# Kernel tuning notes

Measured on AMD Instinct MI355X. Metric: run time of the kernel, lower is better.

The kernel has to match this reference:

```python
import jax, jax.numpy as jnp
import numpy as np
import math

B, L = 512, 32768
NUM_C, NUM_D = 16, 8
RECIPTIVE, STRIDES = 512, 256
EPS = 1e-4


def setup_inputs() -> dict:
    key = jax.random.key(0)
    kx, kw = jax.random.split(key)
    x = jax.random.normal(kx, (B, L), dtype=jnp.float32)
    stdv = 1.0 / math.sqrt(RECIPTIVE)
    weight = jax.random.uniform(kw, (NUM_C, NUM_D, RECIPTIVE), dtype=jnp.float32,
                                minval=-stdv, maxval=stdv)
    return {"x": x, "weight": weight}


def reference(x, weight):
    # x: [B, L], weight: [C, D, R]
    Lx = x.shape[1]
    # sigma = (W W^T + eps I)^{-1} per capsule, [C, D, D]
    wc = jnp.einsum('cdr,cer->cde', weight, weight)
    sigma = jnp.linalg.inv(wc + EPS * jnp.eye(NUM_D, dtype=weight.dtype))
    # circular sliding windows: [W, R] index map (wraparound matches torch.cat branch)
    starts = jnp.arange(0, Lx, STRIDES)
    idx = (starts[:, None] + jnp.arange(RECIPTIVE)[None, :]) % Lx
    windows = x[:, idx]                                   # [B, W, R]
    proj = jnp.einsum('cdr,bwr->bwcd', weight, windows)    # [B, W, C, D]
    q = jnp.einsum('bwcd,cde,bwce->bwc', proj, sigma, proj)  # quadratic form
    return jnp.mean(jnp.sqrt(q), axis=1)                   # [B, C]
```

## Files before the change

### kernel.cpp

```cpp
#include <hip/hip_runtime.h>
#include <hip/hip_bf16.h>

#define NUM_C  16
#define NUM_D  8
#define RECEPT 512
#define LROW   32768
#define EPS_V  1e-4f

#define XCHUNKS 2112
#define XBYTES  (XCHUNKS * 16)

typedef __attribute__((ext_vector_type(8))) short short8;
typedef __attribute__((ext_vector_type(4))) float f32x4;

__device__ __forceinline__ unsigned short f2bf(float f) {
    unsigned int u = __builtin_bit_cast(unsigned int, f);
    u += 0x7fffu + ((u >> 16) & 1u);
    return (unsigned short)(u >> 16);
}

__device__ __forceinline__ int bsw(int a) { return a ^ (((a >> 11) & 7) << 4); }

__device__ __forceinline__ short8 cvt8(f32x4 lo, f32x4 hi) {
    union { short8 s; __hip_bfloat162 h[4]; } u;
    u.h[0] = __float22bfloat162_rn(make_float2(lo[0], lo[1]));
    u.h[1] = __float22bfloat162_rn(make_float2(lo[2], lo[3]));
    u.h[2] = __float22bfloat162_rn(make_float2(hi[0], hi[1]));
    u.h[3] = __float22bfloat162_rn(make_float2(hi[2], hi[3]));
    return u.s;
}

__global__ void prep_kernel(const float* __restrict__ weight,
                            unsigned short* __restrict__ wfrag,
                            float* __restrict__ out) {
    __shared__ float Wc[NUM_D * RECEPT];
    __shared__ float G[NUM_D][NUM_D];
    __shared__ float Lm[NUM_D][NUM_D];
    const int c = blockIdx.x;
    const int t = threadIdx.x;

    out[c * 256 + t] = 0.f;
    out[c * 256 + t + 4096] = 0.f;

    const float4* wsrc4 = reinterpret_cast<const float4*>(
        weight + (size_t)c * NUM_D * RECEPT);
    float4* Wc4 = reinterpret_cast<float4*>(Wc);
    #pragma unroll
    for (int i = 0; i < 4; ++i) Wc4[t + i * 256] = wsrc4[t + i * 256];
    __syncthreads();

    if (t < 64) {
        int d = t >> 3, e = t & 7;
        const float4* wd4 = reinterpret_cast<const float4*>(&Wc[d * RECEPT]);
        const float4* we4 = reinterpret_cast<const float4*>(&Wc[e * RECEPT]);
        float s = 0.f;
        #pragma unroll 4
        for (int r4 = 0; r4 < RECEPT / 4; ++r4) {
            float4 a = wd4[r4], bb = we4[r4];
            s += a.x * bb.x + a.y * bb.y + a.z * bb.z + a.w * bb.w;
        }
        if (d == e) s += EPS_V;
        G[d][e] = s;
    }
    __syncthreads();
    if (t == 0) {
        for (int i = 0; i < NUM_D; ++i) {
            float diag = G[i][i];
            for (int k = 0; k < i; ++k) diag -= Lm[i][k] * Lm[i][k];
            float di = sqrtf(diag);
            Lm[i][i] = di;
            float inv = 1.f / di;
            for (int jj = i + 1; jj < NUM_D; ++jj) {
                float s = G[jj][i];
                for (int k = 0; k < i; ++k) s -= Lm[jj][k] * Lm[i][k];
                Lm[jj][i] = s * inv;
            }
        }
    }
    __syncthreads();
    for (int r = t; r < RECEPT; r += 256) {
        float y[NUM_D];
        for (int d = 0; d < NUM_D; ++d) {
            float s = Wc[d * RECEPT + r];
            for (int k = 0; k < d; ++k) s -= Lm[d][k] * y[k];
            y[d] = s / Lm[d][d];
        }
        const int kk = r >> 5;
        const int g  = (r >> 3) & 3;
        const int j  = r & 7;
        for (int d = 0; d < NUM_D; ++d) {
            int cd = c * NUM_D + d;
            int ntile = cd >> 4;
            int nl = cd & 15;
            int lane = g * 16 + nl;
            int idx = (((ntile * 16 + kk) * 64) + lane) * 8 + j;
            wfrag[idx] = f2bf(y[d]);
        }
    }
}

__global__ __launch_bounds__(256, 4) void main_kernel(
        const float* __restrict__ x,
        const unsigned short* __restrict__ wfrag,
        float* __restrict__ out) {
    __shared__ char lds[XBYTES];
    const int bid = blockIdx.x;
    const int b  = bid >> 2;
    const int qr = bid & 3;
    const int t = threadIdx.x;
    const int lane = t & 63;
    const int wv = t >> 6;
    const int rl = lane & 15;
    const int gl = lane >> 4;
    const int nt0 = wv * 2;

    const char* slice = (const char*)(x + (size_t)b * LROW + qr * 8192);

    #pragma unroll
    for (int i = 0; i < 8; ++i) {
        const int cb = i * 256 + wv * 64;
        const int q = cb + lane;
        const int sq = q ^ ((q >> 7) & 7);
        __builtin_amdgcn_global_load_lds(
            (const __attribute__((address_space(1))) unsigned int*)(slice + sq * 16),
            (__attribute__((address_space(3))) unsigned int*)(lds + cb * 16),
            16, 0, 0);
    }
    if (wv == 0) {
        const char* tsrc = (qr == 3) ? (const char*)(x + (size_t)b * LROW)
                                     : slice + 32768;
        __builtin_amdgcn_global_load_lds(
            (const __attribute__((address_space(1))) unsigned int*)(tsrc + lane * 16),
            (__attribute__((address_space(3))) unsigned int*)(lds + 32768),
            16, 0, 0);
    }

    f32x4 acc[2][2];
    #pragma unroll
    for (int mi = 0; mi < 2; ++mi)
        #pragma unroll
        for (int ni = 0; ni < 2; ++ni)
            acc[mi][ni] = (f32x4){0.f, 0.f, 0.f, 0.f};

    __syncthreads();

    #pragma unroll 1
    for (int q = 0; q < 4; ++q) {
        short8 bq[4][2];
        #pragma unroll
        for (int kkq = 0; kkq < 4; ++kkq)
            #pragma unroll
            for (int ni = 0; ni < 2; ++ni)
                bq[kkq][ni] = *reinterpret_cast<const short8*>(
                    wfrag + ((size_t)(((nt0 + ni) * 16 + q * 4 + kkq) * 64 + lane)) * 8);

        #pragma unroll
        for (int kkq = 0; kkq < 4; ++kkq) {
            short8 af[2];
            #pragma unroll
            for (int mi = 0; mi < 2; ++mi) {
                const int a0 = (mi * 16 + rl) * 1024 + (q * 4 + kkq) * 128 + gl * 32;
                f32x4 lo = *reinterpret_cast<const f32x4*>(lds + bsw(a0));
                f32x4 hi = *reinterpret_cast<const f32x4*>(lds + bsw(a0 + 16));
                af[mi] = cvt8(lo, hi);
            }
            #pragma unroll
            for (int mi = 0; mi < 2; ++mi) {
                acc[mi][0] = __builtin_amdgcn_mfma_f32_16x16x32_bf16(af[mi], bq[kkq][0], acc[mi][0], 0, 0, 0);
                acc[mi][1] = __builtin_amdgcn_mfma_f32_16x16x32_bf16(af[mi], bq[kkq][1], acc[mi][1], 0, 0, 0);
            }
        }
    }

    #pragma unroll
    for (int ni = 0; ni < 2; ++ni) {
        float s = 0.f;
        #pragma unroll
        for (int mi = 0; mi < 2; ++mi) {
            #pragma unroll
            for (int r = 0; r < 4; ++r) {
                float p = acc[mi][ni][r];
                float qq = p * p;
                qq += __shfl_xor(qq, 1);
                qq += __shfl_xor(qq, 2);
                qq += __shfl_xor(qq, 4);
                s += sqrtf(qq);
            }
        }
        s += __shfl_xor(s, 16);
        s += __shfl_xor(s, 32);
        if (lane < 16 && (lane & 7) == 0) {
            int c = (wv * 32 + ni * 16 + lane) >> 3;
            atomicAdd(&out[b * NUM_C + c], s * (1.0f / 128.0f));
        }
    }
}

extern "C" void kernel_launch(void* const* d_in, const int* in_sizes, int n_in,
                              void* d_out, int out_size, void* d_ws, size_t ws_size,
                              hipStream_t stream) {
    (void)in_sizes; (void)n_in; (void)ws_size; (void)out_size;
    const float* x      = (const float*)d_in[0];
    const float* weight = (const float*)d_in[1];
    float* out = (float*)d_out;
    unsigned short* wfrag = (unsigned short*)d_ws;

    prep_kernel<<<16, 256, 0, stream>>>(weight, wfrag, out);
    main_kernel<<<2048, 256, 0, stream>>>(x, wfrag, out);
}
```

Baseline: 39.18 us.

## Persistent blocks with double-buffered LDS prefetch of x slices

The main kernel changes from 2048 one-shot blocks to 512 persistent blocks that each handle four slices. While the current slice is being computed, the next slice is prefetched into a second LDS buffer through global_load_lds, with explicit vmcnt waits and barriers. The aim is to overlap HBM loads with MFMA work across tiles. In exchange, LDS per block doubles, occupancy drops (launch bounds 4 to 2), and the wfrag fragments are still reloaded for every tile.

```diff
diff --git a/kernel.cpp b/kernel.cpp
--- a/kernel.cpp
+++ b/kernel.cpp
@@ -7,8 +7,8 @@
 #define LROW   32768
 #define EPS_V  1e-4f
 
-#define XCHUNKS 2112
-#define XBYTES  (XCHUNKS * 16)
+#define XBYTES  33792
+#define LDS_TOTAL (2 * XBYTES)
 
 typedef __attribute__((ext_vector_type(8))) short short8;
 typedef __attribute__((ext_vector_type(4))) float f32x4;
@@ -99,14 +99,12 @@
     }
 }
 
-__global__ __launch_bounds__(256, 4) void main_kernel(
+__global__ __launch_bounds__(256, 2) void main_kernel(
         const float* __restrict__ x,
         const unsigned short* __restrict__ wfrag,
         float* __restrict__ out) {
-    __shared__ char lds[XBYTES];
+    extern __shared__ char lds[];
     const int bid = blockIdx.x;
-    const int b  = bid >> 2;
-    const int qr = bid & 3;
     const int t = threadIdx.x;
     const int lane = t & 63;
     const int wv = t >> 6;
@@ -114,84 +112,109 @@
     const int gl = lane >> 4;
     const int nt0 = wv * 2;
 
-    const char* slice = (const char*)(x + (size_t)b * LROW + qr * 8192);
-
-    #pragma unroll
-    for (int i = 0; i < 8; ++i) {
-        const int cb = i * 256 + wv * 64;
-        const int q = cb + lane;
-        const int sq = q ^ ((q >> 7) & 7);
-        __builtin_amdgcn_global_load_lds(
-            (const __attribute__((address_space(1))) unsigned int*)(slice + sq * 16),
-            (__attribute__((address_space(3))) unsigned int*)(lds + cb * 16),
-            16, 0, 0);
-    }
-    if (wv == 0) {
-        const char* tsrc = (qr == 3) ? (const char*)(x + (size_t)b * LROW)
-                                     : slice + 32768;
-        __builtin_amdgcn_global_load_lds(
-            (const __attribute__((address_space(1))) unsigned int*)(tsrc + lane * 16),
-            (__attribute__((address_space(3))) unsigned int*)(lds + 32768),
-            16, 0, 0);
-    }
-
-    f32x4 acc[2][2];
-    #pragma unroll
-    for (int mi = 0; mi < 2; ++mi)
+    auto stage = [&](int s, int bufsel) {
+        char* buf = lds + bufsel * XBYTES;
+        const int b = s >> 2, qr = s & 3;
+        const char* slice = (const char*)(x + (size_t)b * LROW + qr * 8192);
         #pragma unroll
-        for (int ni = 0; ni < 2; ++ni)
-            acc[mi][ni] = (f32x4){0.f, 0.f, 0.f, 0.f};
-
-    __syncthreads();
+        for (int i = 0; i < 8; ++i) {
+            const int cb = i * 256 + wv * 64;
+            const int q = cb + lane;
+            const int sq = q ^ ((q >> 7) & 7);
+            __builtin_amdgcn_global_load_lds(
+                (const __attribute__((address_space(1))) unsigned int*)(slice + sq * 16),
+                (__attribute__((address_space(3))) unsigned int*)(buf + cb * 16),
+                16, 0, 0);
+        }
+        if (wv == 0) {
+            const char* tsrc = (qr == 3) ? (const char*)(x + (size_t)b * LROW)
+                                         : slice + 32768;
+            __builtin_amdgcn_global_load_lds(
+                (const __attribute__((address_space(1))) unsigned int*)(tsrc + lane * 16),
+                (__attribute__((address_space(3))) unsigned int*)(buf + 32768),
+                16, 0, 0);
+        }
+    };
+
+    stage(bid, 0);
 
     #pragma unroll 1
-    for (int q = 0; q < 4; ++q) {
-        short8 bq[4][2];
+    for (int tt = 0; tt < 4; ++tt) {
+        const int s = bid + tt * 512;
+
+        if (tt < 3) {
+            stage(s + 512, (tt + 1) & 1);
+            if (wv == 0) asm volatile("s_waitcnt vmcnt(9)" ::: "memory");
+            else         asm volatile("s_waitcnt vmcnt(8)" ::: "memory");
+        } else {
+            asm volatile("s_waitcnt vmcnt(0)" ::: "memory");
+        }
+        __builtin_amdgcn_sched_barrier(0);
+        __builtin_amdgcn_s_barrier();
+        __builtin_amdgcn_sched_barrier(0);
+
+        const char* buf = lds + (tt & 1) * XBYTES;
+
+        f32x4 acc[2][2];
         #pragma unroll
-        for (int kkq = 0; kkq < 4; ++kkq)
+        for (int mi = 0; mi < 2; ++mi)
             #pragma unroll
             for (int ni = 0; ni < 2; ++ni)
-                bq[kkq][ni] = *reinterpret_cast<const short8*>(
-                    wfrag + ((size_t)(((nt0 + ni) * 16 + q * 4 + kkq) * 64 + lane)) * 8);
-
+                acc[mi][ni] = (f32x4){0.f, 0.f, 0.f, 0.f};
+
+        #pragma unroll 1
+        for (int q = 0; q < 4; ++q) {
+            short8 bq[4][2];
+            #pragma unroll
+            for (int kkq = 0; kkq < 4; ++kkq)
+                #pragma unroll
+                for (int ni = 0; ni < 2; ++ni)
+                    bq[kkq][ni] = *reinterpret_cast<const short8*>(
+                        wfrag + ((size_t)(((nt0 + ni) * 16 + q * 4 + kkq) * 64 + lane)) * 8);
+
+            #pragma unroll
+            for (int kkq = 0; kkq < 4; ++kkq) {
+                short8 af[2];
+                #pragma unroll
+                for (int mi = 0; mi < 2; ++mi) {
+                    const int a0 = (mi * 16 + rl) * 1024 + (q * 4 + kkq) * 128 + gl * 32;
+                    f32x4 lo = *reinterpret_cast<const f32x4*>(buf + bsw(a0));
+                    f32x4 hi = *reinterpret_cast<const f32x4*>(buf + bsw(a0 + 16));
+                    af[mi] = cvt8(lo, hi);
+                }
+                #pragma unroll
+                for (int mi = 0; mi < 2; ++mi) {
+                    acc[mi][0] = __builtin_amdgcn_mfma_f32_16x16x32_bf16(af[mi], bq[kkq][0], acc[mi][0], 0, 0, 0);
+                    acc[mi][1] = __builtin_amdgcn_mfma_f32_16x16x32_bf16(af[mi], bq[kkq][1], acc[mi][1], 0, 0, 0);
+                }
+            }
+        }
+        __builtin_amdgcn_sched_barrier(0);
+        __builtin_amdgcn_s_barrier();
+        __builtin_amdgcn_sched_barrier(0);
+
+        const int ob = s >> 2;
         #pragma unroll
-        for (int kkq = 0; kkq < 4; ++kkq) {
-            short8 af[2];
+        for (int ni = 0; ni < 2; ++ni) {
+            float ss = 0.f;
             #pragma unroll
             for (int mi = 0; mi < 2; ++mi) {
-                const int a0 = (mi * 16 + rl) * 1024 + (q * 4 + kkq) * 128 + gl * 32;
-                f32x4 lo = *reinterpret_cast<const f32x4*>(lds + bsw(a0));
-                f32x4 hi = *reinterpret_cast<const f32x4*>(lds + bsw(a0 + 16));
-                af[mi] = cvt8(lo, hi);
-            }
-            #pragma unroll
-            for (int mi = 0; mi < 2; ++mi) {
-                acc[mi][0] = __builtin_amdgcn_mfma_f32_16x16x32_bf16(af[mi], bq[kkq][0], acc[mi][0], 0, 0, 0);
-                acc[mi][1] = __builtin_amdgcn_mfma_f32_16x16x32_bf16(af[mi], bq[kkq][1], acc[mi][1], 0, 0, 0);
-            }
-        }
-    }
-
-    #pragma unroll
-    for (int ni = 0; ni < 2; ++ni) {
-        float s = 0.f;
-        #pragma unroll
-        for (int mi = 0; mi < 2; ++mi) {
-            #pragma unroll
-            for (int r = 0; r < 4; ++r) {
-                float p = acc[mi][ni][r];
-                float qq = p * p;
-                qq += __shfl_xor(qq, 1);
-                qq += __shfl_xor(qq, 2);
-                qq += __shfl_xor(qq, 4);
-                s += sqrtf(qq);
-            }
-        }
-        s += __shfl_xor(s, 16);
-        s += __shfl_xor(s, 32);
-        if (lane < 16 && (lane & 7) == 0) {
-            int c = (wv * 32 + ni * 16 + lane) >> 3;
-            atomicAdd(&out[b * NUM_C + c], s * (1.0f / 128.0f));
+                #pragma unroll
+                for (int r = 0; r < 4; ++r) {
+                    float p = acc[mi][ni][r];
+                    float qq = p * p;
+                    qq += __shfl_xor(qq, 1);
+                    qq += __shfl_xor(qq, 2);
+                    qq += __shfl_xor(qq, 4);
+                    ss += sqrtf(qq);
+                }
+            }
+            ss += __shfl_xor(ss, 16);
+            ss += __shfl_xor(ss, 32);
+            if (lane < 16 && (lane & 7) == 0) {
+                int c = (wv * 32 + ni * 16 + lane) >> 3;
+                atomicAdd(&out[ob * NUM_C + c], ss * (1.0f / 128.0f));
+            }
         }
     }
 }
@@ -206,5 +229,8 @@
     unsigned short* wfrag = (unsigned short*)d_ws;
 
     prep_kernel<<<16, 256, 0, stream>>>(weight, wfrag, out);
-    main_kernel<<<2048, 256, 0, stream>>>(x, wfrag, out);
-}
+
+    hipFuncSetAttribute(reinterpret_cast<const void*>(main_kernel),
+                        hipFuncAttributeMaxDynamicSharedMemorySize, LDS_TOTAL);
+    main_kernel<<<512, 256, LDS_TOTAL, stream>>>(x, wfrag, out);
+}
```

After: 45.12 us. 15.1% more time.

## Convert x to bf16 at staging time and double-buffer weight fragment loads

Applied to the files above, without the earlier changes.

Replaces the direct global-to-LDS float loads with register loads that convert x to bf16 before writing to LDS. This halves the LDS footprint, which should allow more resident blocks, and removes the per-fragment conversion inside the MFMA loop. The weight fragment loads are also double-buffered across the four K quarters so they overlap with compute, and the LDS swizzle is changed to match the bf16 row layout. The cost is that the async LDS load path is lost and the conversion now sits on the critical path before the barrier.

```diff
diff --git a/kernel.cpp b/kernel.cpp
--- a/kernel.cpp
+++ b/kernel.cpp
@@ -7,8 +7,7 @@
 #define LROW   32768
 #define EPS_V  1e-4f
 
-#define XCHUNKS 2112
-#define XBYTES  (XCHUNKS * 16)
+#define XBYTES 16896
 
 typedef __attribute__((ext_vector_type(8))) short short8;
 typedef __attribute__((ext_vector_type(4))) float f32x4;
@@ -19,15 +18,12 @@
     return (unsigned short)(u >> 16);
 }
 
-__device__ __forceinline__ int bsw(int a) { return a ^ (((a >> 11) & 7) << 4); }
-
-__device__ __forceinline__ short8 cvt8(f32x4 lo, f32x4 hi) {
-    union { short8 s; __hip_bfloat162 h[4]; } u;
-    u.h[0] = __float22bfloat162_rn(make_float2(lo[0], lo[1]));
-    u.h[1] = __float22bfloat162_rn(make_float2(lo[2], lo[3]));
-    u.h[2] = __float22bfloat162_rn(make_float2(hi[0], hi[1]));
-    u.h[3] = __float22bfloat162_rn(make_float2(hi[2], hi[3]));
-    return u.s;
+__device__ __forceinline__ int xsw(int a) { return a ^ (((a >> 9) & 7) << 4); }
+
+__device__ __forceinline__ ushort4 cvt4(float4 v) {
+    ushort4 h;
+    h.x = f2bf(v.x); h.y = f2bf(v.y); h.z = f2bf(v.z); h.w = f2bf(v.w);
+    return h;
 }
 
 __global__ void prep_kernel(const float* __restrict__ weight,
@@ -116,24 +112,22 @@
 
     const char* slice = (const char*)(x + (size_t)b * LROW + qr * 8192);
 
-    #pragma unroll
-    for (int i = 0; i < 8; ++i) {
-        const int cb = i * 256 + wv * 64;
-        const int q = cb + lane;
-        const int sq = q ^ ((q >> 7) & 7);
-        __builtin_amdgcn_global_load_lds(
-            (const __attribute__((address_space(1))) unsigned int*)(slice + sq * 16),
-            (__attribute__((address_space(3))) unsigned int*)(lds + cb * 16),
-            16, 0, 0);
-    }
-    if (wv == 0) {
+    float4 va[8], vt;
+    #pragma unroll
+    for (int i = 0; i < 8; ++i)
+        va[i] = *reinterpret_cast<const float4*>(slice + (i * 256 + t) * 16);
+    {
         const char* tsrc = (qr == 3) ? (const char*)(x + (size_t)b * LROW)
                                      : slice + 32768;
-        __builtin_amdgcn_global_load_lds(
-            (const __attribute__((address_space(1))) unsigned int*)(tsrc + lane * 16),
-            (__attribute__((address_space(3))) unsigned int*)(lds + 32768),
-            16, 0, 0);
-    }
+        if (t < 64) vt = *reinterpret_cast<const float4*>(tsrc + t * 16);
+    }
+    #pragma unroll
+    for (int i = 0; i < 8; ++i) {
+        int c8 = (i * 256 + t) * 8;
+        *reinterpret_cast<ushort4*>(lds + xsw(c8)) = cvt4(va[i]);
+    }
+    if (t < 64)
+        *reinterpret_cast<ushort4*>(lds + xsw((2048 + t) * 8)) = cvt4(vt);
 
     f32x4 acc[2][2];
     #pragma unroll
@@ -142,35 +136,41 @@
         for (int ni = 0; ni < 2; ++ni)
             acc[mi][ni] = (f32x4){0.f, 0.f, 0.f, 0.f};
 
-    __syncthreads();
-
-    #pragma unroll 1
-    for (int q = 0; q < 4; ++q) {
-        short8 bq[4][2];
+    short8 bqA[4][2], bqB[4][2];
+    auto loadq = [&](short8 (&dst)[4][2], int q) {
         #pragma unroll
         for (int kkq = 0; kkq < 4; ++kkq)
             #pragma unroll
             for (int ni = 0; ni < 2; ++ni)
-                bq[kkq][ni] = *reinterpret_cast<const short8*>(
+                dst[kkq][ni] = *reinterpret_cast<const short8*>(
                     wfrag + ((size_t)(((nt0 + ni) * 16 + q * 4 + kkq) * 64 + lane)) * 8);
-
+    };
+    auto compute = [&](short8 (&bq)[4][2], int q) {
         #pragma unroll
         for (int kkq = 0; kkq < 4; ++kkq) {
+            const int kb = (q * 4 + kkq) * 64 + gl * 16;
             short8 af[2];
             #pragma unroll
-            for (int mi = 0; mi < 2; ++mi) {
-                const int a0 = (mi * 16 + rl) * 1024 + (q * 4 + kkq) * 128 + gl * 32;
-                f32x4 lo = *reinterpret_cast<const f32x4*>(lds + bsw(a0));
-                f32x4 hi = *reinterpret_cast<const f32x4*>(lds + bsw(a0 + 16));
-                af[mi] = cvt8(lo, hi);
-            }
+            for (int mi = 0; mi < 2; ++mi)
+                af[mi] = *reinterpret_cast<const short8*>(
+                    lds + xsw((mi * 16 + rl) * 512 + kb));
             #pragma unroll
             for (int mi = 0; mi < 2; ++mi) {
                 acc[mi][0] = __builtin_amdgcn_mfma_f32_16x16x32_bf16(af[mi], bq[kkq][0], acc[mi][0], 0, 0, 0);
                 acc[mi][1] = __builtin_amdgcn_mfma_f32_16x16x32_bf16(af[mi], bq[kkq][1], acc[mi][1], 0, 0, 0);
             }
         }
-    }
+    };
+
+    loadq(bqA, 0);
+    loadq(bqB, 1);
+    __syncthreads();
+    compute(bqA, 0);
+    loadq(bqA, 2);
+    compute(bqB, 1);
+    loadq(bqB, 3);
+    compute(bqA, 2);
+    compute(bqB, 3);
 
     #pragma unroll
     for (int ni = 0; ni < 2; ++ni) {
```

Measured after the change: 35.27 us. 1.11x faster.
